# Performance work log

Measured on AMD Instinct MI355X. Metric: run time of the kernel, lower is better.

The kernel has to match this reference:

```python
import jax, jax.numpy as jnp
import numpy as np

DIM, N_HEADS, N_KV, HEAD_DIM = 4096, 32, 8, 128
N_REP = N_HEADS // N_KV
MAX_BS, MAX_SEQ = 2, 2048
ROPE_THETA = 500000.0


def setup_inputs() -> dict:
    key = jax.random.key(0)
    ks = jax.random.split(key, 6)
    b, s = 2, 2048
    x = jax.random.normal(ks[0], (b, s, DIM), dtype=jnp.float32)
    # weights stored like nn.Linear: [out, in]
    sc = 1.0 / np.sqrt(DIM)
    wq = jax.random.normal(ks[1], (N_HEADS * HEAD_DIM, DIM), dtype=jnp.float32) * sc
    wk = jax.random.normal(ks[2], (N_KV * HEAD_DIM, DIM), dtype=jnp.float32) * sc
    wv = jax.random.normal(ks[3], (N_KV * HEAD_DIM, DIM), dtype=jnp.float32) * sc
    wo = jax.random.normal(ks[4], (DIM, N_HEADS * HEAD_DIM), dtype=jnp.float32) * sc
    # rotary tables (real/imag of freq_complex)
    t = jnp.arange(s, dtype=jnp.float32)
    inv = ROPE_THETA ** (-jnp.arange(0, HEAD_DIM, 2, dtype=jnp.float32) / HEAD_DIM)
    ang = t[:, None] * inv[None, :]  # [s, head_dim/2]
    freqs_cos = jnp.cos(ang)
    freqs_sin = jnp.sin(ang)
    cache_k = jnp.zeros((MAX_BS, MAX_SEQ, N_KV, HEAD_DIM), dtype=jnp.float32)
    cache_v = jnp.zeros((MAX_BS, MAX_SEQ, N_KV, HEAD_DIM), dtype=jnp.float32)
    return {"x": x, "wq": wq, "wk": wk, "wv": wv, "wo": wo,
            "freqs_cos": freqs_cos, "freqs_sin": freqs_sin,
            "cache_k": cache_k, "cache_v": cache_v, "start_pos": 0}


def _apply_rope(t, cos, sin):
    # t: [b, s, h, hd]; complex rotation over adjacent pairs
    b, s, h, hd = t.shape
    t2 = t.reshape(b, s, h, hd // 2, 2)
    t0, t1 = t2[..., 0], t2[..., 1]
    c = cos[None, :, None, :]
    sn = sin[None, :, None, :]
    o0 = t0 * c - t1 * sn
    o1 = t0 * sn + t1 * c
    return jnp.stack([o0, o1], axis=-1).reshape(b, s, h, hd)


def reference(x, wq, wk, wv, wo, freqs_cos, freqs_sin, cache_k, cache_v, start_pos):
    b, s, _ = x.shape
    xq = (x @ wq.T).reshape(b, s, N_HEADS, HEAD_DIM)
    xk = (x @ wk.T).reshape(b, s, N_KV, HEAD_DIM)
    xv = (x @ wv.T).reshape(b, s, N_KV, HEAD_DIM)
    xq = _apply_rope(xq, freqs_cos, freqs_sin)
    xk = _apply_rope(xk, freqs_cos, freqs_sin)
    # KV-cache append at start_pos
    cache_k = jax.lax.dynamic_update_slice(cache_k, xk, (0, start_pos, 0, 0))
    cache_v = jax.lax.dynamic_update_slice(cache_v, xv, (0, start_pos, 0, 0))
    kv_len = start_pos + s
    keys = cache_k[:b, :kv_len]   # [b, kv, n_kv, hd]
    vals = cache_v[:b, :kv_len]
    # GQA: group query heads instead of repeating K/V (same math as repeat_kv)
    q = xq.reshape(b, s, N_KV, N_REP, HEAD_DIM)
    scores = jnp.einsum('bsgrd,btgd->bgrst', q, keys) / np.sqrt(HEAD_DIM)
    # causal mask: query i (absolute pos start_pos+i) attends to j <= start_pos+i
    qpos = start_pos + jnp.arange(s)
    kpos = jnp.arange(kv_len)
    mask = kpos[None, :] <= qpos[:, None]  # [s, kv]
    scores = jnp.where(mask[None, None, None], scores, -jnp.inf)
    probs = jax.nn.softmax(scores, axis=-1)
    out = jnp.einsum('bgrst,btgd->bsgrd', probs, vals).reshape(b, s, N_HEADS * HEAD_DIM)
    return out @ wo.T
```

## Files before the change

kernel.cpp:

```cpp
#include <hip/hip_runtime.h>
#include <stdint.h>

typedef unsigned short ushort_t;
typedef short v8s __attribute__((ext_vector_type(8)));
typedef short v4s __attribute__((ext_vector_type(4)));
typedef float v4f __attribute__((ext_vector_type(4)));
typedef unsigned int uint32;

#define DIM   4096
#define NH    32
#define NKV   8
#define HD    128
#define SEQ   2048
#define BATCH 2
#define NTOK  (BATCH * SEQ)
#define QKVN  (NH * HD + 2 * NKV * HD)
#define KOFF  (NH * HD)
#define VOFF  (NH * HD + NKV * HD)

__device__ __forceinline__ ushort_t f2bf(float f) {
    uint32 u = __float_as_uint(f);
    u += 0x7fff + ((u >> 16) & 1);
    return (ushort_t)(u >> 16);
}
__device__ __forceinline__ float bf2f(ushort_t h) {
    return __uint_as_float(((uint32)h) << 16);
}
__device__ __forceinline__ void gl2lds16(const void* g, void* l) {
    __builtin_amdgcn_global_load_lds(
        (const __attribute__((address_space(1))) uint32*)g,
        (__attribute__((address_space(3))) uint32*)l, 16, 0, 0);
}
#if __has_builtin(__builtin_amdgcn_exp2f)
__device__ __forceinline__ float fast_exp2(float x) { return __builtin_amdgcn_exp2f(x); }
#else
__device__ __forceinline__ float fast_exp2(float x) { return exp2f(x); }
#endif

#if !defined(__HIP_DEVICE_COMPILE__)
__host__ __device__ static inline v4f MFMA_B16_K16(v4s a, v4s b, v4f c) {
    (void)a; (void)b; return c;
}
#elif __has_builtin(__builtin_amdgcn_mfma_f32_16x16x16_bf16)
#define MFMA_B16_K16(A, B, C) __builtin_amdgcn_mfma_f32_16x16x16_bf16(A, B, C, 0, 0, 0)
#elif __has_builtin(__builtin_amdgcn_mfma_f32_16x16x16bf16_1k)
#define MFMA_B16_K16(A, B, C) __builtin_amdgcn_mfma_f32_16x16x16bf16_1k(A, B, C, 0, 0, 0)
#else
#error "no 16x16x16 bf16 MFMA builtin on device"
#endif

__global__ void cvt_f32_bf16(const float* __restrict__ src,
                             ushort_t* __restrict__ dst, int n4) {
    int i = blockIdx.x * blockDim.x + threadIdx.x;
    if (i >= n4) return;
    float4 v = ((const float4*)src)[i];
    uint32 lo = ((uint32)f2bf(v.y) << 16) | f2bf(v.x);
    uint32 hi = ((uint32)f2bf(v.w) << 16) | f2bf(v.z);
    ((uint2*)dst)[i] = make_uint2(lo, hi);
}

template <int OUT_BF16>
__global__ __launch_bounds__(512, 2) void gemm_bt8(const ushort_t* __restrict__ A,
                                                   const ushort_t* __restrict__ B,
                                                   float* __restrict__ Cf,
                                                   ushort_t* __restrict__ Cb,
                                                   int M, int N, int K) {
    __shared__ ushort_t sm[2][2][16384];
    const int t = threadIdx.x;
    const int w = t >> 6, lane = t & 63;
    const int g8 = lane >> 4, l16 = lane & 15;
    const int wr = w >> 2, wc = w & 3;

    const int gx = gridDim.x;
    const int nwg = gx * gridDim.y;
    const int wg0 = blockIdx.y * gx + blockIdx.x;
    const int swz = (wg0 & 7) * (nwg >> 3) + (wg0 >> 3);
    const int bm = swz % gx, bn = swz / gx;

    const ushort_t* Ab = A + (size_t)bm * 256 * K;
    const ushort_t* Bb = B + (size_t)bn * 256 * K;

    const int prt = t >> 3;
    const int gg  = (t & 7) ^ (prt & 7);
    const int rA0 = prt,                              rA1 = prt + 128;
    const int rB0 = ((prt >> 5) << 6) + (prt & 31),   rB1 = rB0 + 128;

    const int pgk  = g8 ^ (l16 & 7);
    const int aoff = (wr * 64 + l16) * 64;
    const int boff = (wc * 32 + l16) * 64;

#define STAGE_A(buf, ah, k0)                                                   \
  do {                                                                         \
    gl2lds16(&Ab[(size_t)(rA0 + (ah) * 64) * K + (k0) + gg * 8],               \
             &sm[buf][0][(ah) * 8192 + t * 8]);                                \
    gl2lds16(&Ab[(size_t)(rA1 + (ah) * 64) * K + (k0) + gg * 8],               \
             &sm[buf][0][(ah) * 8192 + 4096 + t * 8]);                         \
  } while (0)
#define STAGE_B(buf, bh, k0)                                                   \
  do {                                                                         \
    gl2lds16(&Bb[(size_t)(rB0 + (bh) * 32) * K + (k0) + gg * 8],               \
             &sm[buf][1][(bh) * 8192 + t * 8]);                                \
    gl2lds16(&Bb[(size_t)(rB1 + (bh) * 32) * K + (k0) + gg * 8],               \
             &sm[buf][1][(bh) * 8192 + 4096 + t * 8]);                         \
  } while (0)
#define LD_A(dst, buf, ihi)                                                    \
  do {                                                                         \
    _Pragma("unroll") for (int i_ = 0; i_ < 4; ++i_) {                         \
      (dst)[i_ * 2 + 0] = *(const v8s*)&sm[buf][0][(ihi) * 8192 + aoff + i_ * 1024 + pgk * 8];       \
      (dst)[i_ * 2 + 1] = *(const v8s*)&sm[buf][0][(ihi) * 8192 + aoff + i_ * 1024 + (pgk ^ 4) * 8]; \
    }                                                                          \
  } while (0)
#define LD_B(dst, buf, jhi)                                                    \
  do {                                                                         \
    _Pragma("unroll") for (int j_ = 0; j_ < 2; ++j_) {                         \
      (dst)[j_ * 2 + 0] = *(const v8s*)&sm[buf][1][(jhi) * 8192 + boff + j_ * 1024 + pgk * 8];       \
      (dst)[j_ * 2 + 1] = *(const v8s*)&sm[buf][1][(jhi) * 8192 + boff + j_ * 1024 + (pgk ^ 4) * 8]; \
    }                                                                          \
  } while (0)
#define MM(IHI, JHI, AF, BF)                                                   \
  do {                                                                         \
    __builtin_amdgcn_s_setprio(1);                                             \
    _Pragma("unroll") for (int k_ = 0; k_ < 2; ++k_)                           \
      _Pragma("unroll") for (int i_ = 0; i_ < 4; ++i_)                         \
        _Pragma("unroll") for (int j_ = 0; j_ < 2; ++j_)                       \
          acc[(IHI) * 4 + i_][(JHI) * 2 + j_] =                                \
              __builtin_amdgcn_mfma_f32_16x16x32_bf16(                         \
                  (AF)[i_ * 2 + k_], (BF)[j_ * 2 + k_],                        \
                  acc[(IHI) * 4 + i_][(JHI) * 2 + j_], 0, 0, 0);               \
    __builtin_amdgcn_s_setprio(0);                                             \
  } while (0)

#define TILE_BODY(T, BF, BL, BH)                                               \
  do {                                                                         \
    const int Tp1 = (T) + 1, Tp2 = (T) + 2;                                    \
              \
    LD_A(af, BF, 0);                                                           \
    LD_B(BH, BF, 1);                                                           \
    if (Tp1 < nk) STAGE_B((BF) ^ 1, 1, Tp1 << 6);                              \
    MM(0, 0, af, BL);                                                          \
    __builtin_amdgcn_s_barrier();                                              \
                                             \
    if (Tp2 < nk) STAGE_A(BF, 0, Tp2 << 6);                                    \
    MM(0, 1, af, BH);                                                          \
    __builtin_amdgcn_s_barrier();                                              \
                                             \
    LD_A(af, BF, 1);                                                           \
    if (Tp2 < nk) STAGE_B(BF, 0, Tp2 << 6);                                    \
    MM(1, 1, af, BH);                                                          \
    __builtin_amdgcn_s_barrier();                                              \
          \
    if (Tp2 < nk) STAGE_A(BF, 1, Tp2 << 6);                                    \
    if ((T) < nk - 2) { asm volatile("s_waitcnt vmcnt(6)" ::: "memory"); }     \
    else              { asm volatile("s_waitcnt vmcnt(0)" ::: "memory"); }     \
    __builtin_amdgcn_s_barrier();                                              \
    if (Tp1 < nk) LD_B(BH, (BF) ^ 1, 0);     \
    MM(1, 0, af, BL);                                                          \
            \
  } while (0)

    v4f acc[8][4];
    v4f z = {0.f, 0.f, 0.f, 0.f};
#pragma unroll
    for (int i = 0; i < 8; i++)
#pragma unroll
        for (int j = 0; j < 4; j++) acc[i][j] = z;
    v8s af[8], b0[4], b1[4];

    const int nk = K >> 6;

    STAGE_A(0, 0, 0);  STAGE_B(0, 0, 0);  STAGE_A(0, 1, 0);  STAGE_B(0, 1, 0);
    STAGE_A(1, 0, 64); STAGE_B(1, 0, 64); STAGE_A(1, 1, 64);
    asm volatile("s_waitcnt vmcnt(6)" ::: "memory");
    __builtin_amdgcn_s_barrier();
    LD_B(b0, 0, 0);

    for (int T = 0; T < nk; T += 2) {
        TILE_BODY(T, 0, b0, b1);
        TILE_BODY(T + 1, 1, b1, b0);
    }

#undef STAGE_A
#undef STAGE_B
#undef LD_A
#undef LD_B
#undef MM
#undef TILE_BODY

    const int rowb = bm * 256 + wr * 128;
    const int colb = bn * 256 + wc * 64;
#pragma unroll
    for (int i = 0; i < 8; i++)
#pragma unroll
        for (int j = 0; j < 4; j++)
#pragma unroll
            for (int r = 0; r < 4; r++) {
                int row = rowb + i * 16 + g8 * 4 + r;
                int col = colb + j * 16 + l16;
                float v = acc[i][j][r];
                if (OUT_BF16)
                    Cb[(size_t)row * N + col] = f2bf(v);
                else
                    Cf[(size_t)row * N + col] = v;
            }
}

__global__ __launch_bounds__(256) void rope_reorg(const ushort_t* __restrict__ qkv,
                                                  const float* __restrict__ fc,
                                                  const float* __restrict__ fs,
                                                  ushort_t* __restrict__ Qo,
                                                  ushort_t* __restrict__ Ko) {
    const int tok = blockIdx.x;
    const int bb = tok >> 11, s = tok & 2047;
    const ushort_t* base = qkv + (size_t)tok * QKVN;
    const int t = threadIdx.x;
    const float qscale = 0.08838834764831845f * 1.4426950408889634f;
    uint32* Qw = (uint32*)Qo;
    uint32* Kw = (uint32*)Ko;
#pragma unroll
    for (int i = 0; i < 8; ++i) {
        int p = i * 256 + t;
        int hh = p >> 6, pi = p & 63;
        float c = fc[s * 64 + pi], sn = fs[s * 64 + pi];
        uint32 u = *(const uint32*)&base[hh * 128 + 2 * pi];
        float t0 = bf2f((ushort_t)(u & 0xffff));
        float t1 = bf2f((ushort_t)(u >> 16));
        float o0 = (t0 * c - t1 * sn) * qscale;
        float o1 = (t0 * sn + t1 * c) * qscale;
        size_t dst = (((size_t)bb * NH + hh) * SEQ + s) * HD + 2 * pi;
        Qw[dst >> 1] = ((uint32)f2bf(o1) << 16) | f2bf(o0);
    }
#pragma unroll
    for (int i = 0; i < 2; ++i) {
        int p = i * 256 + t;
        int hh = p >> 6, pi = p & 63;
        float c = fc[s * 64 + pi], sn = fs[s * 64 + pi];
        uint32 u = *(const uint32*)&base[KOFF + hh * 128 + 2 * pi];
        float t0 = bf2f((ushort_t)(u & 0xffff));
        float t1 = bf2f((ushort_t)(u >> 16));
        float o0 = t0 * c - t1 * sn;
        float o1 = t0 * sn + t1 * c;
        size_t dst = (((size_t)bb * NKV + hh) * SEQ + s) * HD + 2 * pi;
        Kw[dst >> 1] = ((uint32)f2bf(o1) << 16) | f2bf(o0);
    }
}

__global__ __launch_bounds__(256) void v_transpose(const ushort_t* __restrict__ qkv,
                                                   ushort_t* __restrict__ Vt) {
    __shared__ ushort_t tile[64][136];
    const int st = blockIdx.x, kvh = blockIdx.y, bb = blockIdx.z;
    const int t = threadIdx.x;
    const int s0 = st * 64;
#pragma unroll
    for (int i = 0; i < 4; ++i) {
        int c = i * 256 + t;
        int r = c >> 4, col8 = (c & 15) * 8;
        int tok = (bb << 11) + s0 + r;
        *(v8s*)&tile[r][col8] =
            *(const v8s*)&qkv[(size_t)tok * QKVN + VOFF + kvh * 128 + col8];
    }
    __syncthreads();
#pragma unroll
    for (int i = 0; i < 4; ++i) {
        int c = i * 256 + t;
        int d = c >> 3, s8 = (c & 7) * 8;
        ushort_t tmp[8];
#pragma unroll
        for (int j = 0; j < 8; j++) tmp[j] = tile[s8 + j][d];
        *(v8s*)&Vt[(((size_t)bb * NKV + kvh) * HD + d) * SEQ + s0 + s8] =
            *(v8s*)tmp;
    }
}

__global__ __launch_bounds__(256, 4) void attn_kernel(const ushort_t* __restrict__ Q,
                                                      const ushort_t* __restrict__ Kc,
                                                      const ushort_t* __restrict__ Vt,
                                                      ushort_t* __restrict__ Out) {
    __shared__ ushort_t Ks[64 * 128];
    __shared__ ushort_t Vs[128 * 64];
    const int qtb = gridDim.x - 1 - blockIdx.x;
    const int h = blockIdx.y, bb = blockIdx.z;
    const int kvh = h >> 2;
    const int t = threadIdx.x, w = t >> 6, lane = t & 63;
    const int g8 = lane >> 4, l16 = lane & 15;
    const int R = qtb * 64 + w * 16;
    const int qrow = R + l16;

    const size_t qb = (((size_t)bb * NH + h) * SEQ + R) * HD;
    v8s qf[4];
#pragma unroll
    for (int ks = 0; ks < 4; ++ks)
        qf[ks] = *(const v8s*)&Q[qb + (size_t)l16 * HD + ks * 32 + g8 * 8];

    float m_i = -3.0e38f, l_i = 0.f;
    v4f z = {0.f, 0.f, 0.f, 0.f};
    v4f o[8];
#pragma unroll
    for (int n = 0; n < 8; n++) o[n] = z;

    const ushort_t* Kbase = Kc + ((size_t)bb * NKV + kvh) * SEQ * HD;
    const ushort_t* Vbase = Vt + ((size_t)bb * NKV + kvh) * HD * SEQ;

    const int nkt = qtb + 1;
    for (int kt = 0; kt < nkt; ++kt) {
        const int k0 = kt * 64;
        __syncthreads();
        const ushort_t* Kt = Kbase + (size_t)k0 * HD;
#pragma unroll
        for (int i = 0; i < 4; ++i) {
            int c = i * 256 + t;
            int r = c >> 4, cc = (c & 15) ^ (r & 15);
            gl2lds16(&Kt[r * 128 + cc * 8], &Ks[c * 8]);
        }
#pragma unroll
        for (int i = 0; i < 4; ++i) {
            int c = i * 256 + t;
            int d = c >> 3, cc = (c & 7) ^ (d & 7);
            gl2lds16(&Vbase[(size_t)d * SEQ + k0 + cc * 8], &Vs[c * 8]);
        }
        __syncthreads();

        v4f s[4];
#pragma unroll
        for (int j = 0; j < 4; j++) s[j] = z;
#pragma unroll
        for (int j = 0; j < 4; j++)
#pragma unroll
            for (int ks = 0; ks < 4; ks++) {
                const v8s kb = *(const v8s*)&Ks[((j * 16 + l16) * 16 + ((ks * 4 + g8) ^ l16)) * 8];
                s[j] = __builtin_amdgcn_mfma_f32_16x16x32_bf16(kb, qf[ks], s[j], 0, 0, 0);
            }

        if (kt == nkt - 1) {
#pragma unroll
            for (int j = 0; j < 4; j++)
#pragma unroll
                for (int r = 0; r < 4; r++) {
                    int key = k0 + j * 16 + g8 * 4 + r;
                    if (key > qrow) s[j][r] = -3.0e38f;
                }
        }

        float mx = fmaxf(fmaxf(s[0][0], s[0][1]), fmaxf(s[0][2], s[0][3]));
#pragma unroll
        for (int j = 1; j < 4; j++)
            mx = fmaxf(mx, fmaxf(fmaxf(s[j][0], s[j][1]), fmaxf(s[j][2], s[j][3])));
        mx = fmaxf(mx, __shfl_xor(mx, 16, 64));
        mx = fmaxf(mx, __shfl_xor(mx, 32, 64));
        float mnew = fmaxf(m_i, mx);
        float alpha = fast_exp2(m_i - mnew);
        m_i = mnew;

        float sum = 0.f;
        v4s pj[4];
#pragma unroll
        for (int j = 0; j < 4; j++)
#pragma unroll
            for (int r = 0; r < 4; r++) {
                float p = fast_exp2(s[j][r] - m_i);
                sum += p;
                pj[j][r] = (short)f2bf(p);
            }
        sum += __shfl_xor(sum, 16, 64);
        sum += __shfl_xor(sum, 32, 64);
        l_i = l_i * alpha + sum;

        float alo[4];
#pragma unroll
        for (int r = 0; r < 4; r++) alo[r] = __shfl(alpha, g8 * 4 + r, 64);
#pragma unroll
        for (int n = 0; n < 8; n++)
#pragma unroll
            for (int r = 0; r < 4; r++) o[n][r] *= alo[r];

#pragma unroll
        for (int j = 0; j < 4; j++)
#pragma unroll
            for (int n = 0; n < 8; n++) {
                const int d = n * 16 + l16;
                const v4s vb = *(const v4s*)&Vs[d * 64 + (((j * 2 + (g8 >> 1)) ^ (l16 & 7)) * 8) + (g8 & 1) * 4];
                o[n] = MFMA_B16_K16(pj[j], vb, o[n]);
            }
    }

    float lo[4];
#pragma unroll
    for (int r = 0; r < 4; r++) lo[r] = __shfl(l_i, g8 * 4 + r, 64);
#pragma unroll
    for (int n = 0; n < 8; n++)
#pragma unroll
        for (int r = 0; r < 4; r++) {
            int row = R + g8 * 4 + r;
            int col = n * 16 + l16;
            Out[(((size_t)bb * SEQ + row) * NH + h) * HD + col] = f2bf(o[n][r] / lo[r]);
        }
}

extern "C" void kernel_launch(void* const* d_in, const int* in_sizes, int n_in,
                              void* d_out, int out_size, void* d_ws, size_t ws_size,
                              hipStream_t stream) {
    const float* x  = (const float*)d_in[0];
    const float* wq = (const float*)d_in[1];
    const float* wk = (const float*)d_in[2];
    const float* wv = (const float*)d_in[3];
    const float* wo = (const float*)d_in[4];
    const float* fc = (const float*)d_in[5];
    const float* fs = (const float*)d_in[6];
    float* out = (float*)d_out;

    ushort_t* ws = (ushort_t*)d_ws;
    size_t off = 0;
    ushort_t* xb    = ws + off; off += (size_t)NTOK * DIM;
    ushort_t* wqkvb = ws + off; off += (size_t)QKVN * DIM;
    ushort_t* wob   = ws + off; off += (size_t)DIM * DIM;
    ushort_t* qkv   = ws + off; off += (size_t)NTOK * QKVN;
    ushort_t* Qb    = ws + off; off += (size_t)BATCH * NH * SEQ * HD;
    ushort_t* Kb    = ws + off; off += (size_t)BATCH * NKV * SEQ * HD;
    ushort_t* Vt    = ws + off; off += (size_t)BATCH * NKV * HD * SEQ;
    ushort_t* attn_out = xb;

    cvt_f32_bf16<<<(NTOK * DIM / 4) / 256, 256, 0, stream>>>(x, xb, NTOK * DIM / 4);
    cvt_f32_bf16<<<(DIM * DIM / 4) / 256, 256, 0, stream>>>(wq, wqkvb, DIM * DIM / 4);
    cvt_f32_bf16<<<(NKV * HD * DIM / 4) / 256, 256, 0, stream>>>(
        wk, wqkvb + (size_t)KOFF * DIM, NKV * HD * DIM / 4);
    cvt_f32_bf16<<<(NKV * HD * DIM / 4) / 256, 256, 0, stream>>>(
        wv, wqkvb + (size_t)VOFF * DIM, NKV * HD * DIM / 4);
    cvt_f32_bf16<<<(DIM * DIM / 4) / 256, 256, 0, stream>>>(wo, wob, DIM * DIM / 4);

    dim3 g1(NTOK / 256, QKVN / 256);
    gemm_bt8<1><<<g1, 512, 0, stream>>>(xb, wqkvb, nullptr, qkv, NTOK, QKVN, DIM);

    rope_reorg<<<NTOK, 256, 0, stream>>>(qkv, fc, fs, Qb, Kb);
    dim3 gv(SEQ / 64, NKV, BATCH);
    v_transpose<<<gv, 256, 0, stream>>>(qkv, Vt);

    dim3 ga(SEQ / 64, NH, BATCH);
    attn_kernel<<<ga, 256, 0, stream>>>(Qb, Kb, Vt, attn_out);

    dim3 g2(NTOK / 256, DIM / 256);
    gemm_bt8<0><<<g2, 512, 0, stream>>>(attn_out, wob, out, nullptr, NTOK, DIM, DIM);
}
```

Before: 807.4 us.

## Double-buffer K/V tiles in attention and enlarge query tile to 128 rows

The attention kernel now runs 512 threads per block over 128 query rows, so each K/V tile loaded into LDS serves eight waves instead of four. K/V tiles are double-buffered: the next tile is loaded asynchronously while the current one is computed, using a partial vmcnt wait and raw barriers instead of two full syncthreads per iteration. MFMA sections are wrapped in s_setprio to favour matrix issue. The trade-off is twice the LDS per block (64KB), which may lower occupancy, plus half as many blocks, which can worsen load balance across the causal triangle.

```diff
diff --git a/kernel.cpp b/kernel.cpp
--- a/kernel.cpp
+++ b/kernel.cpp
@@ -271,18 +271,18 @@
     }
 }
 
-__global__ __launch_bounds__(256, 4) void attn_kernel(const ushort_t* __restrict__ Q,
+__global__ __launch_bounds__(512, 4) void attn_kernel(const ushort_t* __restrict__ Q,
                                                       const ushort_t* __restrict__ Kc,
                                                       const ushort_t* __restrict__ Vt,
                                                       ushort_t* __restrict__ Out) {
-    __shared__ ushort_t Ks[64 * 128];
-    __shared__ ushort_t Vs[128 * 64];
+    __shared__ ushort_t Ks[2][64 * 128];
+    __shared__ ushort_t Vs[2][128 * 64];
     const int qtb = gridDim.x - 1 - blockIdx.x;
     const int h = blockIdx.y, bb = blockIdx.z;
     const int kvh = h >> 2;
     const int t = threadIdx.x, w = t >> 6, lane = t & 63;
     const int g8 = lane >> 4, l16 = lane & 15;
-    const int R = qtb * 64 + w * 16;
+    const int R = qtb * 128 + w * 16;
     const int qrow = R + l16;
 
     const size_t qb = (((size_t)bb * NH + h) * SEQ + R) * HD;
@@ -300,37 +300,49 @@
     const ushort_t* Kbase = Kc + ((size_t)bb * NKV + kvh) * SEQ * HD;
     const ushort_t* Vbase = Vt + ((size_t)bb * NKV + kvh) * HD * SEQ;
 
-    const int nkt = qtb + 1;
+#define STAGE_KV(bf, kt)                                                       \
+  do {                                                                         \
+    const ushort_t* Kt_ = Kbase + (size_t)(kt) * 64 * HD;                      \
+    _Pragma("unroll") for (int i_ = 0; i_ < 2; ++i_) {                         \
+      int c_ = i_ * 512 + t;                                                   \
+      int r_ = c_ >> 4, cc_ = (c_ & 15) ^ (r_ & 15);                           \
+      gl2lds16(&Kt_[r_ * 128 + cc_ * 8], &Ks[bf][c_ * 8]);                     \
+    }                                                                          \
+    _Pragma("unroll") for (int i_ = 0; i_ < 2; ++i_) {                         \
+      int c_ = i_ * 512 + t;                                                   \
+      int d_ = c_ >> 3, cc_ = (c_ & 7) ^ (d_ & 7);                             \
+      gl2lds16(&Vbase[(size_t)d_ * SEQ + (kt) * 64 + cc_ * 8],                 \
+               &Vs[bf][c_ * 8]);                                               \
+    }                                                                          \
+  } while (0)
+
+    const int nkt = 2 * qtb + 2;
+    STAGE_KV(0, 0);
     for (int kt = 0; kt < nkt; ++kt) {
+        const int bf = kt & 1;
         const int k0 = kt * 64;
-        __syncthreads();
-        const ushort_t* Kt = Kbase + (size_t)k0 * HD;
-#pragma unroll
-        for (int i = 0; i < 4; ++i) {
-            int c = i * 256 + t;
-            int r = c >> 4, cc = (c & 15) ^ (r & 15);
-            gl2lds16(&Kt[r * 128 + cc * 8], &Ks[c * 8]);
+        if (kt + 1 < nkt) {
+            STAGE_KV(bf ^ 1, kt + 1);
+            asm volatile("s_waitcnt vmcnt(4)" ::: "memory");
+        } else {
+            asm volatile("s_waitcnt vmcnt(0)" ::: "memory");
         }
-#pragma unroll
-        for (int i = 0; i < 4; ++i) {
-            int c = i * 256 + t;
-            int d = c >> 3, cc = (c & 7) ^ (d & 7);
-            gl2lds16(&Vbase[(size_t)d * SEQ + k0 + cc * 8], &Vs[c * 8]);
-        }
-        __syncthreads();
+        __builtin_amdgcn_s_barrier();
 
         v4f s[4];
 #pragma unroll
         for (int j = 0; j < 4; j++) s[j] = z;
+        __builtin_amdgcn_s_setprio(1);
 #pragma unroll
         for (int j = 0; j < 4; j++)
 #pragma unroll
             for (int ks = 0; ks < 4; ks++) {
-                const v8s kb = *(const v8s*)&Ks[((j * 16 + l16) * 16 + ((ks * 4 + g8) ^ l16)) * 8];
+                const v8s kb = *(const v8s*)&Ks[bf][((j * 16 + l16) * 16 + ((ks * 4 + g8) ^ l16)) * 8];
                 s[j] = __builtin_amdgcn_mfma_f32_16x16x32_bf16(kb, qf[ks], s[j], 0, 0, 0);
             }
-
-        if (kt == nkt - 1) {
+        __builtin_amdgcn_s_setprio(0);
+
+        if (kt >= 2 * qtb) {
 #pragma unroll
             for (int j = 0; j < 4; j++)
 #pragma unroll
@@ -372,15 +384,20 @@
 #pragma unroll
             for (int r = 0; r < 4; r++) o[n][r] *= alo[r];
 
+        __builtin_amdgcn_s_setprio(1);
 #pragma unroll
         for (int j = 0; j < 4; j++)
 #pragma unroll
             for (int n = 0; n < 8; n++) {
                 const int d = n * 16 + l16;
-                const v4s vb = *(const v4s*)&Vs[d * 64 + (((j * 2 + (g8 >> 1)) ^ (l16 & 7)) * 8) + (g8 & 1) * 4];
+                const v4s vb = *(const v4s*)&Vs[bf][d * 64 + (((j * 2 + (g8 >> 1)) ^ (l16 & 7)) * 8) + (g8 & 1) * 4];
                 o[n] = MFMA_B16_K16(pj[j], vb, o[n]);
             }
-    }
+        __builtin_amdgcn_s_setprio(0);
+
+        __builtin_amdgcn_s_barrier();
+    }
+#undef STAGE_KV
 
     float lo[4];
 #pragma unroll
@@ -433,8 +450,8 @@
     dim3 gv(SEQ / 64, NKV, BATCH);
     v_transpose<<<gv, 256, 0, stream>>>(qkv, Vt);
 
-    dim3 ga(SEQ / 64, NH, BATCH);
-    attn_kernel<<<ga, 256, 0, stream>>>(Qb, Kb, Vt, attn_out);
+    dim3 ga(SEQ / 128, NH, BATCH);
+    attn_kernel<<<ga, 512, 0, stream>>>(Qb, Kb, Vt, attn_out);
 
     dim3 g2(NTOK / 256, DIM / 256);
     gemm_bt8<0><<<g2, 512, 0, stream>>>(attn_out, wob, out, nullptr, NTOK, DIM, DIM);
```

After: 790.1 us. -2.1%, faster.
